# Performance work log

Measured on AMD Instinct MI355X. Metric: run time of the kernel, lower is better.

The kernel has to match this reference:

```python
import jax, jax.numpy as jnp
import numpy as np

K = 20
EPS = 1e-5
NEG_SLOPE = 0.2


def _bn(x, gamma, beta, axes):
    # batch-norm in training mode (batch statistics), per-channel on last axis
    mean = jnp.mean(x, axis=axes, keepdims=True)
    var = jnp.var(x, axis=axes, keepdims=True)
    return gamma * (x - mean) * jax.lax.rsqrt(var + EPS) + beta


def _lrelu(x):
    return jnp.where(x >= 0, x, NEG_SLOPE * x)


def setup_inputs() -> dict:
    key = jax.random.key(0)
    ks = jax.random.split(key, 8)
    B, C, N = 8, 6, 4096

    def w(k_, shape):
        fan_in = shape[-1]
        return jax.random.normal(k_, shape, jnp.float32) / np.sqrt(fan_in)

    return {
        "x": jax.random.normal(ks[0], (B, C, N), jnp.float32),
        "conv1_w": w(ks[1], (64, 12)),
        "bn1_g": jnp.ones((64,), jnp.float32), "bn1_b": jnp.zeros((64,), jnp.float32),
        "conv2_w": w(ks[2], (128, 64)),
        "bn2_g": jnp.ones((128,), jnp.float32), "bn2_b": jnp.zeros((128,), jnp.float32),
        "conv3_w": w(ks[3], (1024, 128)),
        "bn3_g": jnp.ones((1024,), jnp.float32), "bn3_b": jnp.zeros((1024,), jnp.float32),
        "fc1_w": w(ks[4], (512, 1024)),
        "bn4_g": jnp.ones((512,), jnp.float32), "bn4_b": jnp.zeros((512,), jnp.float32),
        "fc2_w": w(ks[5], (256, 512)),
        "bn5_g": jnp.ones((256,), jnp.float32), "bn5_b": jnp.zeros((256,), jnp.float32),
        "fc3_w": w(ks[6], (9, 256)), "fc3_b": jnp.zeros((9,), jnp.float32),
        "fc4_w": w(ks[7], (3, 256)), "fc4_b": jnp.zeros((3,), jnp.float32),
    }


def _get_graph_feature(x, k):
    # x: [B, C, N] -> [B, N, k, 2C]
    B, C, N = x.shape
    xt = jnp.transpose(x, (0, 2, 1))                      # [B, N, C]
    xx = jnp.sum(xt * xt, axis=-1)                        # [B, N]
    inner = jnp.einsum('bnc,bmc->bnm', xt, xt)            # [B, N, N]
    pd = 2.0 * inner - xx[:, :, None] - xx[:, None, :]    # -||xi-xj||^2
    _, idx = jax.lax.top_k(pd, k)                         # [B, N, k]
    nbr = xt[jnp.arange(B)[:, None, None], idx]           # [B, N, k, C]
    center = jnp.broadcast_to(xt[:, :, None, :], nbr.shape)
    return jnp.concatenate([nbr - center, center], axis=-1)  # [B, N, k, 2C]


def reference(x, conv1_w, bn1_g, bn1_b, conv2_w, bn2_g, bn2_b,
              conv3_w, bn3_g, bn3_b, fc1_w, bn4_g, bn4_b,
              fc2_w, bn5_g, bn5_b, fc3_w, fc3_b, fc4_w, fc4_b):
    B = x.shape[0]
    feat = _get_graph_feature(x, K)                            # [B, N, k, 12]
    h = _lrelu(_bn(jnp.einsum('bnkc,oc->bnko', feat, conv1_w), bn1_g, bn1_b, (0, 1, 2)))
    h = _lrelu(_bn(jnp.einsum('bnkc,oc->bnko', h, conv2_w), bn2_g, bn2_b, (0, 1, 2)))
    h = jnp.max(h, axis=2)                                     # [B, N, 128] max over k
    h = _lrelu(_bn(jnp.einsum('bnc,oc->bno', h, conv3_w), bn3_g, bn3_b, (0, 1)))
    g = jnp.max(h, axis=1)                                     # [B, 1024] max over points
    g = _lrelu(_bn(g @ fc1_w.T, bn4_g, bn4_b, (0,)))           # [B, 512]
    g = _lrelu(_bn(g @ fc2_w.T, bn5_g, bn5_b, (0,)))           # [B, 256]
    bias = (g @ fc4_w.T + fc4_b)[:, None, :]                   # [B, 1, 3]
    matrix = jnp.eye(3, dtype=x.dtype) + (g @ fc3_w.T + fc3_b).reshape(B, 3, 3)
    xyz = jnp.transpose(x[:, :3, :], (0, 2, 1))                # [B, N, 3]
    out = jnp.einsum('bnc,bcd->bnd', xyz, matrix) + bias       # [B, N, 3]
    return jnp.transpose(out, (0, 2, 1))                       # [B, 3, N]
```

## Files before the change

kernel.cpp:

```cpp
#include <hip/hip_runtime.h>
#include <math.h>
#include <stddef.h>


static constexpr float EPS_ = 1e-5f;

__global__ __launch_bounds__(256) void k_prep(const float* __restrict__ x,
                                              float* __restrict__ xtp)
{
    int i = blockIdx.x*256 + threadIdx.x;
    int b = i >> 12, n = i & 4095;
    const float* xb = x + (size_t)b*6*4096 + n;
    float v0 = xb[0], v1 = xb[4096], v2 = xb[2*4096];
    float v3 = xb[3*4096], v4 = xb[4*4096], v5 = xb[5*4096];
    float xx = v0*v0 + v1*v1 + v2*v2 + v3*v3 + v4*v4 + v5*v5;
    float4* o = (float4*)(xtp + (size_t)i*8);
    o[0] = make_float4(v0, v1, v2, v3);
    o[1] = make_float4(v4, v5, xx, 0.f);
}

__device__ __forceinline__ float pd_calc(const float4 a0, const float4 a1,
                                         const float4 q0, const float4 q1)
{
    float dot = a0.x*q0.x;
    dot = fmaf(a0.y, q0.y, dot);
    dot = fmaf(a0.z, q0.z, dot);
    dot = fmaf(a0.w, q0.w, dot);
    dot = fmaf(a1.x, q1.x, dot);
    dot = fmaf(a1.y, q1.y, dot);
    return fmaf(2.f, dot, -a1.z - q1.z);
}

#define TK_CAP 384
__global__ __launch_bounds__(256) void k_topk(const float* __restrict__ xtp,
                                              int* __restrict__ idxout)
{
    __shared__ float maxs[4][256];
    __shared__ float candv[4][TK_CAP];
    __shared__ int   candi[4][TK_CAP];
    __shared__ float Ts[4];
    __shared__ unsigned ccnt[4];

    const int t = threadIdx.x;
    const int rowbase = blockIdx.x << 2;
    const int b = rowbase >> 12;
    const float* xb = xtp + ((size_t)b << 15);

    float4 c0[4], c1[4];
    #pragma unroll
    for (int c = 0; c < 4; c++){
        const float4* p = (const float4*)(xtp + (size_t)(rowbase + c)*8);
        c0[c] = p[0]; c1[c] = p[1];
    }

    float mx[4] = {-INFINITY, -INFINITY, -INFINITY, -INFINITY};
    for (int i = 0; i < 16; i++){
        const float4* p = (const float4*)(xb + (size_t)((i << 8) | t)*8);
        float4 q0 = p[0], q1 = p[1];
        #pragma unroll
        for (int c = 0; c < 4; c++)
            mx[c] = fmaxf(mx[c], pd_calc(c0[c], c1[c], q0, q1));
    }
    #pragma unroll
    for (int c = 0; c < 4; c++) maxs[c][t] = mx[c];
    if (t < 4) ccnt[t] = 0u;
    __syncthreads();

    const int w = t >> 6, lane = t & 63;
    {
        float v[4];
        #pragma unroll
        for (int j = 0; j < 4; j++) v[j] = maxs[w][(j << 6) | lane];
        float gv = -INFINITY;
        for (int r = 0; r < 20; r++){
            float bv = fmaxf(fmaxf(v[0], v[1]), fmaxf(v[2], v[3]));
            gv = bv;
            #pragma unroll
            for (int s = 1; s < 64; s <<= 1) gv = fmaxf(gv, __shfl_xor(gv, s));
            if (bv == gv){
                if      (v[0] == gv) v[0] = -INFINITY;
                else if (v[1] == gv) v[1] = -INFINITY;
                else if (v[2] == gv) v[2] = -INFINITY;
                else                 v[3] = -INFINITY;
            }
        }
        if (lane == 0) Ts[w] = gv;
    }
    __syncthreads();

    #pragma unroll
    for (int c = 0; c < 4; c++){
        if (mx[c] >= Ts[c]){
            float Tc = Ts[c];
            for (int i = 0; i < 16; i++){
                int m = (i << 8) | t;
                const float4* p = (const float4*)(xb + (size_t)m*8);
                float4 q0 = p[0], q1 = p[1];
                float pd = pd_calc(c0[c], c1[c], q0, q1);
                if (pd >= Tc){
                    unsigned pos = atomicAdd(&ccnt[c], 1u);
                    if (pos < TK_CAP){ candv[c][pos] = pd; candi[c][pos] = m; }
                }
            }
        }
    }
    __syncthreads();

    {
        int n = (int)min(ccnt[w], (unsigned)TK_CAP);
        float v[6]; int id[6];
        #pragma unroll
        for (int j = 0; j < 6; j++){
            int p = (j << 6) | lane;
            bool ok = p < n;
            v[j]  = ok ? candv[w][p] : -INFINITY;
            id[j] = ok ? candi[w][p] : 0x7fffffff;
        }
        int* out = idxout + (size_t)(rowbase + w)*20;
        for (int r = 0; r < 20; r++){
            float bv = -INFINITY; int bi = 0x7fffffff, bj = 0;
            #pragma unroll
            for (int j = 0; j < 6; j++){
                bool better = (v[j] > bv) || (v[j] == bv && id[j] < bi);
                if (better){ bv = v[j]; bi = id[j]; bj = j; }
            }
            float gv = bv; int gi = bi;
            #pragma unroll
            for (int s = 1; s < 64; s <<= 1){
                float ov = __shfl_xor(gv, s); int oi = __shfl_xor(gi, s);
                if (ov > gv || (ov == gv && oi < gi)){ gv = ov; gi = oi; }
            }
            if (lane == 0) out[r] = (gi == 0x7fffffff) ? 0 : gi;
            if (bi == gi){ v[bj] = -INFINITY; id[bj] = 0x7fffffff; }
        }
    }
}

__global__ __launch_bounds__(256) void k_bn1stats(const float* __restrict__ xtp,
                                                  const int* __restrict__ idxb,
                                                  const float* __restrict__ w1,
                                                  float* __restrict__ bn1sum,
                                                  float* __restrict__ bn1sq)
{
    __shared__ float fT[320*12];
    __shared__ float red[2][4][64];
    const int t = threadIdx.x;
    const int rowbase = blockIdx.x << 4;
    const int b = rowbase >> 12;

    for (int s = t; s < 320; s += 256){
        int r = s / 20, k = s % 20;
        int grow = rowbase + r;
        int m = idxb[(size_t)grow*20 + k];
        const float4* pn = (const float4*)(xtp + (size_t)((b << 12) | m)*8);
        const float4* pc = (const float4*)(xtp + (size_t)grow*8);
        float4 n0 = pn[0], n1 = pn[1], c0 = pc[0], c1 = pc[1];
        float* f = fT + s*12;
        ((float4*)f)[0] = make_float4(n0.x-c0.x, n0.y-c0.y, n0.z-c0.z, n0.w-c0.w);
        ((float4*)f)[1] = make_float4(n1.x-c1.x, n1.y-c1.y, c0.x, c0.y);
        ((float4*)f)[2] = make_float4(c0.z, c0.w, c1.x, c1.y);
    }
    __syncthreads();
    const int o = t & 63, grp = t >> 6;
    float w[12];
    #pragma unroll
    for (int c = 0; c < 12; c++) w[c] = w1[o*12 + c];
    float sm = 0.f, sq = 0.f;
    for (int s = grp*80; s < grp*80 + 80; s++){
        const float* f = fT + s*12;
        float4 f0 = *(const float4*)(f);
        float4 fa = *(const float4*)(f + 4);
        float4 fb = *(const float4*)(f + 8);
        float h = w[0]*f0.x + w[1]*f0.y + w[2]*f0.z + w[3]*f0.w
                + w[4]*fa.x + w[5]*fa.y + w[6]*fa.z + w[7]*fa.w
                + w[8]*fb.x + w[9]*fb.y + w[10]*fb.z + w[11]*fb.w;
        sm += h; sq = fmaf(h, h, sq);
    }
    red[0][grp][o] = sm; red[1][grp][o] = sq;
    __syncthreads();
    if (t < 64){
        float a = red[0][0][t] + red[0][1][t] + red[0][2][t] + red[0][3][t];
        float c2 = red[1][0][t] + red[1][1][t] + red[1][2][t] + red[1][3][t];
        atomicAdd(bn1sum + t, a);
        atomicAdd(bn1sq + t, c2);
    }
}

__global__ void k_bnfin(const float* __restrict__ sum, const float* __restrict__ sq,
                        const float* __restrict__ gamma, const float* __restrict__ beta,
                        float* __restrict__ st, int C, float invN)
{
    int o = threadIdx.x;
    if (o < C){
        float mean = sum[o]*invN;
        float var  = sq[o]*invN - mean*mean;
        float s = gamma[o]/sqrtf(var + EPS_);
        st[o] = s;
        st[C + o] = beta[o] - mean*s;
    }
}

__global__ __launch_bounds__(256) void k_conv12(
    const float* __restrict__ xtp, const int* __restrict__ idxb,
    const float* __restrict__ w1, const float* __restrict__ w2,
    const float* __restrict__ bn1st,
    float* __restrict__ h2max, float* __restrict__ bn2sum, float* __restrict__ bn2sq)
{
    __shared__ float fT[4*20*12];
    __shared__ float f1s[4*20*64];
    __shared__ float w2t[64*132];
    __shared__ float w1s[64*13];
    const int t = threadIdx.x;
    const int rowbase = blockIdx.x << 2;
    const int b = rowbase >> 12;

    for (int e = t; e < 64*12; e += 256) w1s[(e/12)*13 + (e%12)] = w1[e];
    for (int e = t; e < 128*64; e += 256) w2t[(e & 63)*132 + (e >> 6)] = w2[e];
    if (t < 80){
        int r = t / 20, k = t % 20;
        int grow = rowbase + r;
        int m = idxb[(size_t)grow*20 + k];
        const float4* pn = (const float4*)(xtp + (size_t)((b << 12) | m)*8);
        const float4* pc = (const float4*)(xtp + (size_t)grow*8);
        float4 n0 = pn[0], n1 = pn[1], c0 = pc[0], c1 = pc[1];
        float* f = fT + (r*20 + k)*12;
        ((float4*)f)[0] = make_float4(n0.x-c0.x, n0.y-c0.y, n0.z-c0.z, n0.w-c0.w);
        ((float4*)f)[1] = make_float4(n1.x-c1.x, n1.y-c1.y, c0.x, c0.y);
        ((float4*)f)[2] = make_float4(c0.z, c0.w, c1.x, c1.y);
    }
    __syncthreads();
    {
        const int j = t & 63;
        const float s1 = bn1st[j], t1 = bn1st[64 + j];
        float wr[12];
        #pragma unroll
        for (int c = 0; c < 12; c++) wr[c] = w1s[j*13 + c];
        for (int vid = t; vid < 4*20*64; vid += 256){
            const float* f = fT + (vid >> 6)*12;
            float4 f0 = *(const float4*)(f);
            float4 fa = *(const float4*)(f + 4);
            float4 fb = *(const float4*)(f + 8);
            float acc = wr[0]*f0.x + wr[1]*f0.y + wr[2]*f0.z + wr[3]*f0.w
                      + wr[4]*fa.x + wr[5]*fa.y + wr[6]*fa.z + wr[7]*fa.w
                      + wr[8]*fb.x + wr[9]*fb.y + wr[10]*fb.z + wr[11]*fb.w;
            float v = fmaf(s1, acc, t1);
            f1s[vid] = fmaxf(v, 0.2f*v);
        }
    }
    __syncthreads();
    const int oq = t & 31, kslot = t >> 5;
    const int o0 = oq << 2;
    float mx[4][4], sm[4][4], sq[4][4];
    #pragma unroll
    for (int r = 0; r < 4; r++)
        #pragma unroll
        for (int i = 0; i < 4; i++){ mx[r][i] = -INFINITY; sm[r][i] = 0.f; sq[r][i] = 0.f; }
    for (int k = kslot; k < 20; k += 8){
        float h[4][4];
        #pragma unroll
        for (int r = 0; r < 4; r++){ h[r][0]=0.f; h[r][1]=0.f; h[r][2]=0.f; h[r][3]=0.f; }
        for (int j = 0; j < 64; j += 4){
            float wv[4][4];
            #pragma unroll
            for (int jj = 0; jj < 4; jj++)
                *(float4*)wv[jj] = *(const float4*)&w2t[(j + jj)*132 + o0];
            #pragma unroll
            for (int r = 0; r < 4; r++){
                float fv[4];
                *(float4*)fv = *(const float4*)&f1s[((r*20 + k) << 6) + j];
                #pragma unroll
                for (int jj = 0; jj < 4; jj++)
                    #pragma unroll
                    for (int oi = 0; oi < 4; oi++)
                        h[r][oi] = fmaf(fv[jj], wv[jj][oi], h[r][oi]);
            }
        }
        #pragma unroll
        for (int r = 0; r < 4; r++)
            #pragma unroll
            for (int oi = 0; oi < 4; oi++){
                mx[r][oi] = fmaxf(mx[r][oi], h[r][oi]);
                sm[r][oi] += h[r][oi];
                sq[r][oi] = fmaf(h[r][oi], h[r][oi], sq[r][oi]);
            }
    }
    __syncthreads();
    #pragma unroll
    for (int r = 0; r < 4; r++)
        *(float4*)&f1s[((kslot << 2) + r)*128 + o0] = make_float4(mx[r][0], mx[r][1], mx[r][2], mx[r][3]);
    __syncthreads();
    for (int it = t; it < 512; it += 256){
        int r = it >> 7, o = it & 127;
        float m = f1s[r*128 + o];
        #pragma unroll
        for (int ks = 1; ks < 8; ks++) m = fmaxf(m, f1s[((ks << 2) + r)*128 + o]);
        h2max[(size_t)(rowbase + r)*128 + o] = m;
    }
    __syncthreads();
    #pragma unroll
    for (int r = 0; r < 4; r++)
        *(float4*)&f1s[((kslot << 2) + r)*128 + o0] = make_float4(sm[r][0], sm[r][1], sm[r][2], sm[r][3]);
    __syncthreads();
    if (t < 128){
        float s = 0.f;
        #pragma unroll
        for (int i = 0; i < 32; i++) s += f1s[i*128 + t];
        atomicAdd(bn2sum + t, s);
    }
    __syncthreads();
    #pragma unroll
    for (int r = 0; r < 4; r++)
        *(float4*)&f1s[((kslot << 2) + r)*128 + o0] = make_float4(sq[r][0], sq[r][1], sq[r][2], sq[r][3]);
    __syncthreads();
    if (t < 128){
        float s = 0.f;
        #pragma unroll
        for (int i = 0; i < 32; i++) s += f1s[i*128 + t];
        atomicAdd(bn2sq + t, s);
    }
}

__global__ __launch_bounds__(256) void k_conv3(const float* __restrict__ h2max,
    const float* __restrict__ bn2st, const float* __restrict__ w3,
    float* __restrict__ bn3sum, float* __restrict__ bn3sq, unsigned int* __restrict__ gkey)
{
    __shared__ float f2[32*132];
    __shared__ float w3t[128*68];
    const int t = threadIdx.x;
    const int rt = blockIdx.x >> 4;
    const int ot = blockIdx.x & 15;
    const int rowbase = rt << 5;
    const int obase = ot << 6;
    const int b = rowbase >> 12;

    for (int e = t; e < 32*128; e += 256){
        int r = e >> 7, c = e & 127;
        float v = h2max[(size_t)(rowbase + r)*128 + c];
        float u = fmaf(bn2st[c], v, bn2st[128 + c]);
        f2[r*132 + c] = fmaxf(u, 0.2f*u);
    }
    for (int e = t; e < 64*128; e += 256){
        int ol = e >> 7, j = e & 127;
        w3t[j*68 + ol] = w3[(size_t)(obase + ol)*128 + j];
    }
    __syncthreads();
    const int oq = t & 15, rg = t >> 4;
    const int o0 = oq << 2, r0 = rg << 1;
    float h0[4] = {0.f,0.f,0.f,0.f}, h1[4] = {0.f,0.f,0.f,0.f};
    for (int j = 0; j < 128; j += 4){
        float wv[4][4];
        #pragma unroll
        for (int jj = 0; jj < 4; jj++)
            *(float4*)wv[jj] = *(const float4*)&w3t[(j + jj)*68 + o0];
        float fa[4], fb[4];
        *(float4*)fa = *(const float4*)&f2[r0*132 + j];
        *(float4*)fb = *(const float4*)&f2[(r0 + 1)*132 + j];
        #pragma unroll
        for (int jj = 0; jj < 4; jj++)
            #pragma unroll
            for (int oi = 0; oi < 4; oi++){
                h0[oi] = fmaf(fa[jj], wv[jj][oi], h0[oi]);
                h1[oi] = fmaf(fb[jj], wv[jj][oi], h1[oi]);
            }
    }
    __syncthreads();
    float* scratch = f2;
    *(float4*)&scratch[(rg << 6) + o0] =
        make_float4(h0[0]+h1[0], h0[1]+h1[1], h0[2]+h1[2], h0[3]+h1[3]);
    __syncthreads();
    if (t < 64){
        float s = 0.f;
        #pragma unroll
        for (int g2 = 0; g2 < 16; g2++) s += scratch[(g2 << 6) + t];
        atomicAdd(bn3sum + obase + t, s);
    }
    __syncthreads();
    *(float4*)&scratch[(rg << 6) + o0] =
        make_float4(h0[0]*h0[0]+h1[0]*h1[0], h0[1]*h0[1]+h1[1]*h1[1],
                    h0[2]*h0[2]+h1[2]*h1[2], h0[3]*h0[3]+h1[3]*h1[3]);
    __syncthreads();
    if (t < 64){
        float s = 0.f;
        #pragma unroll
        for (int g2 = 0; g2 < 16; g2++) s += scratch[(g2 << 6) + t];
        atomicAdd(bn3sq + obase + t, s);
    }
    __syncthreads();
    *(float4*)&scratch[(rg << 6) + o0] =
        make_float4(fmaxf(h0[0],h1[0]), fmaxf(h0[1],h1[1]),
                    fmaxf(h0[2],h1[2]), fmaxf(h0[3],h1[3]));
    __syncthreads();
    if (t < 64){
        float m = scratch[t];
        #pragma unroll
        for (int g2 = 1; g2 < 16; g2++) m = fmaxf(m, scratch[(g2 << 6) + t]);
        unsigned u = __float_as_uint(m);
        unsigned key = (u & 0x80000000u) ? ~u : (u | 0x80000000u);
        atomicMax(gkey + (b << 10) + obase + t, key);
    }
}

__global__ void k_bn3g(const float* __restrict__ sum, const float* __restrict__ sq,
                       const unsigned int* __restrict__ gkey,
                       const float* __restrict__ gamma, const float* __restrict__ beta,
                       float* __restrict__ g)
{
    int o = blockIdx.x*256 + threadIdx.x;
    if (o < 1024){
        float mean = sum[o]*(1.f/32768.f);
        float var  = sq[o]*(1.f/32768.f) - mean*mean;
        float s = gamma[o]/sqrtf(var + EPS_);
        float tt = beta[o] - mean*s;
        for (int b = 0; b < 8; b++){
            unsigned k = gkey[(b << 10) + o];
            unsigned u = (k & 0x80000000u) ? (k & 0x7fffffffu) : ~k;
            float v = __uint_as_float(u);
            float xv = fmaf(s, v, tt);
            g[(b << 10) + o] = fmaxf(xv, 0.2f*xv);
        }
    }
}

__global__ __launch_bounds__(256) void k_fc(const float* __restrict__ in,
                                            const float* __restrict__ w,
                                            float* __restrict__ out, int Kdim, int Odim)
{
    int wid = (blockIdx.x*256 + threadIdx.x) >> 6;
    int lane = threadIdx.x & 63;
    int nout = 8*Odim;
    if (wid >= nout) return;
    int b = wid / Odim, o = wid - b*Odim;
    const float* gi = in + (size_t)b*Kdim;
    const float* wr = w + (size_t)o*Kdim;
    float acc = 0.f;
    for (int c = lane; c < Kdim; c += 64) acc = fmaf(gi[c], wr[c], acc);
    #pragma unroll
    for (int s = 32; s > 0; s >>= 1) acc += __shfl_xor(acc, s);
    if (lane == 0) out[(size_t)b*Odim + o] = acc;
}

__global__ void k_bnb(const float* __restrict__ h, const float* __restrict__ gamma,
                      const float* __restrict__ beta, float* __restrict__ g, int C)
{
    int o = blockIdx.x*256 + threadIdx.x;
    if (o < C){
        float s = 0.f, q = 0.f;
        for (int b = 0; b < 8; b++){ float v = h[(size_t)b*C + o]; s += v; q = fmaf(v, v, q); }
        float mean = s*0.125f;
        float var  = q*0.125f - mean*mean;
        float sc = gamma[o]/sqrtf(var + EPS_);
        float tt = beta[o] - mean*sc;
        for (int b = 0; b < 8; b++){
            float xv = fmaf(sc, h[(size_t)b*C + o], tt);
            g[(size_t)b*C + o] = fmaxf(xv, 0.2f*xv);
        }
    }
}

__global__ void k_head(const float* __restrict__ g5,
                       const float* __restrict__ fc3w, const float* __restrict__ fc3b,
                       const float* __restrict__ fc4w, const float* __restrict__ fc4b,
                       float* __restrict__ mat, float* __restrict__ bias3)
{
    int t = threadIdx.x;
    if (t < 96){
        int b = t / 12, j = t % 12;
        const float* gi = g5 + b*256;
        if (j < 9){
            const float* w = fc3w + j*256;
            float a = fc3b[j];
            for (int c = 0; c < 256; c++) a = fmaf(gi[c], w[c], a);
            if (j == 0 || j == 4 || j == 8) a += 1.f;
            mat[b*9 + j] = a;
        } else {
            int d = j - 9;
            const float* w = fc4w + d*256;
            float a = fc4b[d];
            for (int c = 0; c < 256; c++) a = fmaf(gi[c], w[c], a);
            bias3[b*3 + d] = a;
        }
    }
}

__global__ __launch_bounds__(256) void k_out(const float* __restrict__ x,
                                             const float* __restrict__ mat,
                                             const float* __restrict__ bias3,
                                             float* __restrict__ out)
{
    int i = blockIdx.x*256 + threadIdx.x;
    int n = i & 4095, bd = i >> 12;
    int b = bd / 3, d = bd - b*3;
    const float* xb = x + (size_t)b*6*4096 + n;
    const float* M = mat + b*9;
    out[i] = xb[0]*M[d] + xb[4096]*M[3 + d] + xb[2*4096]*M[6 + d] + bias3[b*3 + d];
}

extern "C" void kernel_launch(void* const* d_in, const int* in_sizes, int n_in,
                              void* d_out, int out_size, void* d_ws, size_t ws_size,
                              hipStream_t stream)
{
    const float* x     = (const float*)d_in[0];
    const float* w1    = (const float*)d_in[1];
    const float* bn1g  = (const float*)d_in[2];
    const float* bn1b  = (const float*)d_in[3];
    const float* w2    = (const float*)d_in[4];
    const float* bn2g  = (const float*)d_in[5];
    const float* bn2b  = (const float*)d_in[6];
    const float* w3    = (const float*)d_in[7];
    const float* bn3gm = (const float*)d_in[8];
    const float* bn3bt = (const float*)d_in[9];
    const float* fc1w  = (const float*)d_in[10];
    const float* bn4g  = (const float*)d_in[11];
    const float* bn4b  = (const float*)d_in[12];
    const float* fc2w  = (const float*)d_in[13];
    const float* bn5g  = (const float*)d_in[14];
    const float* bn5b  = (const float*)d_in[15];
    const float* fc3w  = (const float*)d_in[16];
    const float* fc3b  = (const float*)d_in[17];
    const float* fc4w  = (const float*)d_in[18];
    const float* fc4b  = (const float*)d_in[19];
    float* out = (float*)d_out;

    char* ws = (char*)d_ws;
    float* xtp   = (float*)(ws);
    int*   idxb  = (int*)  (ws + 1048576);
    float* h2max = (float*)(ws + 3670016);
    float* zs    = (float*)(ws + 20447232);
    float* bn1sum = zs;            float* bn1sq = zs + 64;
    float* bn2sum = zs + 128;      float* bn2sq = zs + 256;
    float* bn3sum = zs + 384;      float* bn3sq = zs + 1408;
    unsigned int* gkey = (unsigned int*)(zs + 2432);
    float* tail  = (float*)(ws + 20489728);
    float* bn1st = tail;
    float* bn2st = tail + 128;
    float* g     = tail + 384;
    float* h4    = tail + 8576;
    float* g4    = tail + 12672;
    float* h5    = tail + 16768;
    float* g5    = tail + 18816;
    float* mat   = tail + 20864;
    float* bias3 = tail + 20936;

    hipMemsetAsync(zs, 0, 42496, stream);

    k_prep    <<<128,   256, 0, stream>>>(x, xtp);
    k_topk    <<<8192,  256, 0, stream>>>(xtp, idxb);
    k_bn1stats<<<2048,  256, 0, stream>>>(xtp, idxb, w1, bn1sum, bn1sq);
    k_bnfin   <<<1,     128, 0, stream>>>(bn1sum, bn1sq, bn1g, bn1b, bn1st, 64, 1.f/655360.f);
    k_conv12  <<<8192,  256, 0, stream>>>(xtp, idxb, w1, w2, bn1st, h2max, bn2sum, bn2sq);
    k_bnfin   <<<1,     128, 0, stream>>>(bn2sum, bn2sq, bn2g, bn2b, bn2st, 128, 1.f/655360.f);
    k_conv3   <<<16384, 256, 0, stream>>>(h2max, bn2st, w3, bn3sum, bn3sq, gkey);
    k_bn3g    <<<4,     256, 0, stream>>>(bn3sum, bn3sq, gkey, bn3gm, bn3bt, g);
    k_fc      <<<1024,  256, 0, stream>>>(g, fc1w, h4, 1024, 512);
    k_bnb     <<<2,     256, 0, stream>>>(h4, bn4g, bn4b, g4, 512);
    k_fc      <<<512,   256, 0, stream>>>(g4, fc2w, h5, 512, 256);
    k_bnb     <<<1,     256, 0, stream>>>(h5, bn5g, bn5b, g5, 256);
    k_head    <<<1,     128, 0, stream>>>(g5, fc3w, fc3b, fc4w, fc4b, mat, bias3);
    k_out     <<<384,   256, 0, stream>>>(x, mat, bias3, out);
}
```

Before: 805.2 us.

## Pretranspose conv2/conv3 weights once in global memory, read directly instead of staging in LDS

```diff
diff --git a/kernel.cpp b/kernel.cpp
--- a/kernel.cpp
+++ b/kernel.cpp
@@ -6,7 +6,9 @@
 static constexpr float EPS_ = 1e-5f;
 
 __global__ __launch_bounds__(256) void k_prep(const float* __restrict__ x,
-                                              float* __restrict__ xtp)
+                                              float* __restrict__ xtp,
+                                              const float* __restrict__ w2,
+                                              float* __restrict__ w2t)
 {
     int i = blockIdx.x*256 + threadIdx.x;
     int b = i >> 12, n = i & 4095;
@@ -17,6 +19,13 @@
     float4* o = (float4*)(xtp + (size_t)i*8);
     o[0] = make_float4(v0, v1, v2, v3);
     o[1] = make_float4(v4, v5, xx, 0.f);
+    if (blockIdx.x < 2){
+        int e = blockIdx.x*256 + threadIdx.x;
+        for (int q = e; q < 64*128; q += 512){
+            int c = q >> 7, oo = q & 127;
+            w2t[q] = w2[oo*64 + c];
+        }
+    }
 }
 
 __device__ __forceinline__ float pd_calc(const float4 a0, const float4 a1,
@@ -200,22 +209,20 @@
     }
 }
 
-__global__ __launch_bounds__(256) void k_conv12(
+__global__ __launch_bounds__(256, 5) void k_conv12(
     const float* __restrict__ xtp, const int* __restrict__ idxb,
-    const float* __restrict__ w1, const float* __restrict__ w2,
+    const float* __restrict__ w1, const float* __restrict__ w2t,
     const float* __restrict__ bn1st,
     float* __restrict__ h2max, float* __restrict__ bn2sum, float* __restrict__ bn2sq)
 {
     __shared__ float fT[4*20*12];
     __shared__ float f1s[4*20*64];
-    __shared__ float w2t[64*132];
     __shared__ float w1s[64*13];
     const int t = threadIdx.x;
     const int rowbase = blockIdx.x << 2;
     const int b = rowbase >> 12;
 
     for (int e = t; e < 64*12; e += 256) w1s[(e/12)*13 + (e%12)] = w1[e];
-    for (int e = t; e < 128*64; e += 256) w2t[(e & 63)*132 + (e >> 6)] = w2[e];
     if (t < 80){
         int r = t / 20, k = t % 20;
         int grow = rowbase + r;
@@ -250,6 +257,7 @@
     __syncthreads();
     const int oq = t & 31, kslot = t >> 5;
     const int o0 = oq << 2;
+    const float* w2p = w2t + o0;
     float mx[4][4], sm[4][4], sq[4][4];
     #pragma unroll
     for (int r = 0; r < 4; r++)
@@ -263,7 +271,7 @@
             float wv[4][4];
             #pragma unroll
             for (int jj = 0; jj < 4; jj++)
-                *(float4*)wv[jj] = *(const float4*)&w2t[(j + jj)*132 + o0];
+                *(float4*)wv[jj] = *(const float4*)&w2p[(j + jj)*128];
             #pragma unroll
             for (int r = 0; r < 4; r++){
                 float fv[4];
@@ -320,12 +328,19 @@
     }
 }
 
-__global__ __launch_bounds__(256) void k_conv3(const float* __restrict__ h2max,
-    const float* __restrict__ bn2st, const float* __restrict__ w3,
+__global__ __launch_bounds__(256) void k_wt3(const float* __restrict__ w3,
+                                             float* __restrict__ w3t)
+{
+    int i = blockIdx.x*256 + threadIdx.x;
+    int j = i >> 10, o = i & 1023;
+    w3t[i] = w3[(size_t)o*128 + j];
+}
+
+__global__ __launch_bounds__(256, 5) void k_conv3(const float* __restrict__ h2max,
+    const float* __restrict__ bn2st, const float* __restrict__ w3t,
     float* __restrict__ bn3sum, float* __restrict__ bn3sq, unsigned int* __restrict__ gkey)
 {
     __shared__ float f2[32*132];
-    __shared__ float w3t[128*68];
     const int t = threadIdx.x;
     const int rt = blockIdx.x >> 4;
     const int ot = blockIdx.x & 15;
@@ -339,19 +354,16 @@
         float u = fmaf(bn2st[c], v, bn2st[128 + c]);
         f2[r*132 + c] = fmaxf(u, 0.2f*u);
     }
-    for (int e = t; e < 64*128; e += 256){
-        int ol = e >> 7, j = e & 127;
-        w3t[j*68 + ol] = w3[(size_t)(obase + ol)*128 + j];
-    }
     __syncthreads();
     const int oq = t & 15, rg = t >> 4;
     const int o0 = oq << 2, r0 = rg << 1;
+    const float* w3p = w3t + obase + o0;
     float h0[4] = {0.f,0.f,0.f,0.f}, h1[4] = {0.f,0.f,0.f,0.f};
     for (int j = 0; j < 128; j += 4){
         float wv[4][4];
         #pragma unroll
         for (int jj = 0; jj < 4; jj++)
-            *(float4*)wv[jj] = *(const float4*)&w3t[(j + jj)*68 + o0];
+            *(float4*)wv[jj] = *(const float4*)&w3p[(size_t)(j + jj)*1024];
         float fa[4], fb[4];
         *(float4*)fa = *(const float4*)&f2[r0*132 + j];
         *(float4*)fb = *(const float4*)&f2[(r0 + 1)*132 + j];
@@ -523,6 +535,7 @@
 
     char* ws = (char*)d_ws;
     float* xtp   = (float*)(ws);
+    float* w3t_g = (float*)(ws);
     int*   idxb  = (int*)  (ws + 1048576);
     float* h2max = (float*)(ws + 3670016);
     float* zs    = (float*)(ws + 20447232);
@@ -540,16 +553,18 @@
     float* g5    = tail + 18816;
     float* mat   = tail + 20864;
     float* bias3 = tail + 20936;
+    float* w2t_g = (float*)(ws + 20573568);
 
     hipMemsetAsync(zs, 0, 42496, stream);
 
-    k_prep    <<<128,   256, 0, stream>>>(x, xtp);
+    k_prep    <<<128,   256, 0, stream>>>(x, xtp, w2, w2t_g);
     k_topk    <<<8192,  256, 0, stream>>>(xtp, idxb);
     k_bn1stats<<<2048,  256, 0, stream>>>(xtp, idxb, w1, bn1sum, bn1sq);
     k_bnfin   <<<1,     128, 0, stream>>>(bn1sum, bn1sq, bn1g, bn1b, bn1st, 64, 1.f/655360.f);
-    k_conv12  <<<8192,  256, 0, stream>>>(xtp, idxb, w1, w2, bn1st, h2max, bn2sum, bn2sq);
+    k_conv12  <<<8192,  256, 0, stream>>>(xtp, idxb, w1, w2t_g, bn1st, h2max, bn2sum, bn2sq);
+    k_wt3     <<<512,   256, 0, stream>>>(w3, w3t_g);
     k_bnfin   <<<1,     128, 0, stream>>>(bn2sum, bn2sq, bn2g, bn2b, bn2st, 128, 1.f/655360.f);
-    k_conv3   <<<16384, 256, 0, stream>>>(h2max, bn2st, w3, bn3sum, bn3sq, gkey);
+    k_conv3   <<<16384, 256, 0, stream>>>(h2max, bn2st, w3t_g, bn3sum, bn3sq, gkey);
     k_bn3g    <<<4,     256, 0, stream>>>(bn3sum, bn3sq, gkey, bn3gm, bn3bt, g);
     k_fc      <<<1024,  256, 0, stream>>>(g, fc1w, h4, 1024, 512);
     k_bnb     <<<2,     256, 0, stream>>>(h4, bn4g, bn4b, g4, 512);
```

Result: slower. 899.7 us (+11.7%).
